# Kernel optimization log

Measured on AMD Instinct MI355X. Metric: run time of the kernel, lower is better.

The kernel has to match this reference:

```python
import jax, jax.numpy as jnp
import numpy as np

B, N, D, H = 1, 4096, 768, 12
HD = D // H
SCALE = HD ** -0.5

def setup_inputs() -> dict:
    key = jax.random.key(0)
    k1, k2, k3 = jax.random.split(key, 3)
    x = jax.random.normal(k1, (B, N, D), dtype=jnp.float32)
    W_qkv = jax.random.normal(k2, (D, 3 * D), dtype=jnp.float32) * (D ** -0.5)
    W_out = jax.random.normal(k3, (D, D), dtype=jnp.float32) * (D ** -0.5)
    b_out = jnp.zeros((D,), dtype=jnp.float32)
    return {"x": x, "W_qkv": W_qkv, "W_out": W_out, "b_out": b_out}

def reference(x, W_qkv, W_out, b_out):
    # qkv projection: (B,N,3D)
    qkv = x @ W_qkv
    q, k, v = jnp.split(qkv, 3, axis=-1)
    # (B,N,D) -> (B,H,N,hd)
    def heads(t):
        return t.reshape(B, N, H, HD).transpose(0, 2, 1, 3)
    q, k, v = heads(q), heads(k), heads(v)
    scores = jnp.einsum('bhnd,bhmd->bhnm', q, k) * SCALE  # (B,H,N,N)
    attn = jax.nn.softmax(scores, axis=-1)
    out = jnp.einsum('bhnm,bhmd->bhnd', attn, v)
    out = out.transpose(0, 2, 1, 3).reshape(B, N, D)
    return out @ W_out + b_out
```

## Files before the change

kernel.cpp:

```cpp
#include <hip/hip_runtime.h>
#include <hip/hip_bf16.h>
#include <math.h>

typedef __attribute__((ext_vector_type(8))) short bf16x8;
typedef __attribute__((ext_vector_type(4))) short bf16x4;
typedef __attribute__((ext_vector_type(4))) float floatx4;

constexpr int kN  = 4096;
constexpr int kD  = 768;
constexpr int kH  = 12;
constexpr int kHD = 64;
constexpr int k3D = 2304;
constexpr float kQScale = 0.18033688011112042f;

static __device__ __forceinline__ short f2b(float f) {
    __hip_bfloat16 h = __float2bfloat16(f);
    return *reinterpret_cast<short*>(&h);
}

static __device__ __forceinline__ float fast_exp2(float x) {
#if __has_builtin(__builtin_amdgcn_exp2f)
    return __builtin_amdgcn_exp2f(x);
#else
    return exp2f(x);
#endif
}

static __device__ __forceinline__ void async_copy16(const void* g, void* l) {
    __builtin_amdgcn_global_load_lds(
        (const __attribute__((address_space(1))) void*)g,
        (__attribute__((address_space(3))) void*)l, 16, 0, 0);
}

constexpr int kBlkX  = 1536;
constexpr int kBlkWq = 72 * 24;
constexpr int kBlkWo = 24 * 24;

__global__ __launch_bounds__(256)
void prep(const float* __restrict__ x, const float* __restrict__ Wq,
          const float* __restrict__ Wo, short* __restrict__ Xb,
          short* __restrict__ WqT, short* __restrict__ WoT)
{
    const int bid = blockIdx.x;
    const int tid = threadIdx.x;
    if (bid < kBlkX) {
        const int i = bid * 256 + tid;
        const float4* s = reinterpret_cast<const float4*>(x + (size_t)i * 8);
        float4 a = s[0], b = s[1];
        bf16x8 v;
        v[0] = f2b(a.x); v[1] = f2b(a.y); v[2] = f2b(a.z); v[3] = f2b(a.w);
        v[4] = f2b(b.x); v[5] = f2b(b.y); v[6] = f2b(b.z); v[7] = f2b(b.w);
        *reinterpret_cast<bf16x8*>(Xb + (size_t)i * 8) = v;
        return;
    }
    const float* src; short* dst; int R, C, bx, by;
    if (bid < kBlkX + kBlkWq) {
        const int local = bid - kBlkX;
        src = Wq; dst = WqT; R = kD; C = k3D; bx = local % 72; by = local / 72;
    } else {
        const int local = bid - kBlkX - kBlkWq;
        src = Wo; dst = WoT; R = kD; C = kD; bx = local % 24; by = local / 24;
    }
    __shared__ float t[32][33];
    const int c0 = bx * 32, r0 = by * 32;
    const int tx = tid & 31, ty = tid >> 5;
    #pragma unroll
    for (int i = ty; i < 32; i += 8)
        t[i][tx] = src[(size_t)(r0 + i) * C + c0 + tx];
    __syncthreads();
    #pragma unroll
    for (int i = ty; i < 32; i += 8)
        dst[(size_t)(c0 + i) * R + r0 + tx] = f2b(t[tx][i]);
}

template<int MODE>
__device__ __forceinline__
void gemm_core(const short* __restrict__ A, const short* __restrict__ BT,
               const float* __restrict__ bias, float* __restrict__ Cout,
               short* __restrict__ Qh, short* __restrict__ Kh, short* __restrict__ Vt,
               int N, int K)
{
    const int bm   = blockIdx.x * 128;
    const int bn   = blockIdx.y * 128;
    const int tid  = threadIdx.x;
    const int wave = tid >> 6;
    const int lane = tid & 63;
    const int l15  = lane & 15;
    const int quad = lane >> 4;
    const int l3   = l15 & 3;

    __shared__ alignas(16) short As[128 * 32];
    __shared__ alignas(16) short Bs[128 * 32];

    floatx4 acc[4][4] = {};
    const int wm = (wave >> 1) * 64;
    const int wn = (wave & 1) * 64;

    const int srl = lane >> 2;
    const int scc = (lane & 3) ^ (srl & 3);

    for (int k0 = 0; k0 < K; k0 += 32) {
        __syncthreads();
        #pragma unroll
        for (int j = 0; j < 2; ++j) {
            const int rs = 32 * wave + 16 * j;
            async_copy16(&A [(size_t)(bm + rs + srl) * K + k0 + 8 * scc], &As[rs * 32]);
            async_copy16(&BT[(size_t)(bn + rs + srl) * K + k0 + 8 * scc], &Bs[rs * 32]);
        }
        __syncthreads();

        bf16x8 af[4], bfr[4];
        #pragma unroll
        for (int mt = 0; mt < 4; ++mt)
            af[mt] = *reinterpret_cast<const bf16x8*>(&As[(wm + 16 * mt + l15) * 32 + 8 * (quad ^ l3)]);
        #pragma unroll
        for (int nt = 0; nt < 4; ++nt)
            bfr[nt] = *reinterpret_cast<const bf16x8*>(&Bs[(wn + 16 * nt + l15) * 32 + 8 * (quad ^ l3)]);
        #pragma unroll
        for (int mt = 0; mt < 4; ++mt)
            #pragma unroll
            for (int nt = 0; nt < 4; ++nt)
                acc[mt][nt] = __builtin_amdgcn_mfma_f32_16x16x32_bf16(af[mt], bfr[nt], acc[mt][nt], 0, 0, 0);
    }

    #pragma unroll
    for (int mt = 0; mt < 4; ++mt) {
        #pragma unroll
        for (int nt = 0; nt < 4; ++nt) {
            #pragma unroll
            for (int r = 0; r < 4; ++r) {
                const int row = bm + wm + mt * 16 + 4 * quad + r;
                const int col = bn + wn + nt * 16 + l15;
                float v = acc[mt][nt][r];
                if (MODE == 0) {
                    Cout[(size_t)row * N + col] = v + bias[col];
                } else {
                    const int proj   = col / kD;
                    const int within = col - proj * kD;
                    const int h = within >> 6;
                    const int d = within & 63;
                    if (proj == 0)      Qh[((size_t)h * kN + row) * kHD + d] = f2b(v * kQScale);
                    else if (proj == 1) Kh[((size_t)h * kN + row) * kHD + d] = f2b(v);
                    else                Vt[((size_t)h * kHD + d) * kN + row] = f2b(v);
                }
            }
        }
    }
}

__global__ __launch_bounds__(256)
void gemm_qkv(const short* __restrict__ A, const short* __restrict__ BT,
              short* __restrict__ Qh, short* __restrict__ Kh, short* __restrict__ Vt)
{
    gemm_core<1>(A, BT, nullptr, nullptr, Qh, Kh, Vt, k3D, kD);
}

__global__ __launch_bounds__(256)
void gemm_out(const short* __restrict__ A, const short* __restrict__ BT,
              const float* __restrict__ bias, float* __restrict__ Cout)
{
    gemm_core<0>(A, BT, bias, Cout, nullptr, nullptr, nullptr, kD, kD);
}

__global__ __launch_bounds__(256)
void attn(const short* __restrict__ Qh, const short* __restrict__ Kh,
          const short* __restrict__ Vt, short* __restrict__ AO)
{
    const int h    = blockIdx.y;
    const int q0   = blockIdx.x * 64;
    const int tid  = threadIdx.x;
    const int wave = tid >> 6;
    const int lane = tid & 63;
    const int l15  = lane & 15;
    const int quad = lane >> 4;
    const int lx   = l15 & 7;

    __shared__ alignas(16) short Ks[128 * 64];
    __shared__ alignas(16) short Vs[64 * 128];
    __shared__ alignas(16) short Pm[4 * 2048];

    const int qrow = q0 + 16 * wave + l15;
    const size_t qbase = ((size_t)h * kN + qrow) * kHD;
    bf16x8 qf[2];
    qf[0] = *reinterpret_cast<const bf16x8*>(&Qh[qbase + quad * 8]);
    qf[1] = *reinterpret_cast<const bf16x8*>(&Qh[qbase + 32 + quad * 8]);

    floatx4 oacc[4] = {};
    float psum = 0.f;

    const int krl = lane >> 3;
    const int kcc = (lane & 7) ^ (krl & 7);
    const int vrl = lane >> 4;
    const int vp  = lane & 15;

    short* Pw = Pm + wave * 2048;

    for (int kv0 = 0; kv0 < kN; kv0 += 128) {
        __syncthreads();
        #pragma unroll
        for (int j = 0; j < 4; ++j) {
            const int rk = 32 * wave + 8 * j;
            async_copy16(&Kh[((size_t)h * kN + kv0 + rk + krl) * kHD + 8 * kcc],
                         &Ks[rk * 64]);
            const int rv0 = 16 * wave + 4 * j;
            const int rv  = rv0 + vrl;
            async_copy16(&Vt[((size_t)h * kHD + rv) * kN + kv0 + 8 * (vp ^ (rv & 7))],
                         &Vs[rv0 * 128]);
        }
        __syncthreads();

        floatx4 sacc[8] = {};
        #pragma unroll
        for (int nt = 0; nt < 8; ++nt) {
            #pragma unroll
            for (int s = 0; s < 2; ++s) {
                bf16x8 kf = *reinterpret_cast<const bf16x8*>(
                    &Ks[(16 * nt + l15) * 64 + 8 * ((4 * s + quad) ^ lx)]);
                sacc[nt] = __builtin_amdgcn_mfma_f32_16x16x32_bf16(kf, qf[s], sacc[nt], 0, 0, 0);
            }
        }

        #pragma unroll
        for (int nt = 0; nt < 8; ++nt) {
            const float p0 = fast_exp2(sacc[nt][0]);
            const float p1 = fast_exp2(sacc[nt][1]);
            const float p2 = fast_exp2(sacc[nt][2]);
            const float p3 = fast_exp2(sacc[nt][3]);
            psum += (p0 + p1) + (p2 + p3);
            bf16x4 pk;
            pk[0] = f2b(p0); pk[1] = f2b(p1); pk[2] = f2b(p2); pk[3] = f2b(p3);
            const int c = 2 * nt + (quad >> 1);
            *reinterpret_cast<bf16x4*>(
                &Pw[l15 * 128 + 8 * (c ^ l15) + 4 * (quad & 1)]) = pk;
        }

        #pragma unroll
        for (int s = 0; s < 4; ++s) {
            bf16x8 pa = *reinterpret_cast<const bf16x8*>(
                &Pw[l15 * 128 + 8 * ((4 * s + quad) ^ l15)]);
            #pragma unroll
            for (int dt = 0; dt < 4; ++dt) {
                bf16x8 vv = *reinterpret_cast<const bf16x8*>(
                    &Vs[(16 * dt + l15) * 128 + 8 * ((4 * s + quad) ^ lx)]);
                oacc[dt] = __builtin_amdgcn_mfma_f32_16x16x32_bf16(pa, vv, oacc[dt], 0, 0, 0);
            }
        }
    }

    float v = psum;
    v += __shfl_xor(v, 16);
    v += __shfl_xor(v, 32);
    float lrow[4];
    #pragma unroll
    for (int r = 0; r < 4; ++r)
        lrow[r] = __shfl(v, 4 * quad + r);

    #pragma unroll
    for (int dt = 0; dt < 4; ++dt) {
        #pragma unroll
        for (int r = 0; r < 4; ++r) {
            const int row = q0 + 16 * wave + 4 * quad + r;
            const int col = h * kHD + 16 * dt + l15;
            AO[(size_t)row * kD + col] = f2b(oacc[dt][r] / lrow[r]);
        }
    }
}

extern "C" void kernel_launch(void* const* d_in, const int* in_sizes, int n_in,
                              void* d_out, int out_size, void* d_ws, size_t ws_size,
                              hipStream_t stream)
{
    const float* x     = (const float*)d_in[0];
    const float* W_qkv = (const float*)d_in[1];
    const float* W_out = (const float*)d_in[2];
    const float* b_out = (const float*)d_in[3];
    float* out = (float*)d_out;

    const size_t HNHD = (size_t)kH * kN * kHD;
    short* Qh    = (short*)d_ws;
    short* Kh    = Qh + HNHD;
    short* Vt    = Kh + HNHD;
    short* Xb    = Vt + HNHD;
    short* WqkvT = Xb + (size_t)kN * kD;
    short* WoutT = WqkvT + (size_t)k3D * kD;
    short* AO    = Xb;
    (void)in_sizes; (void)n_in; (void)out_size; (void)ws_size;

    prep<<<dim3(kBlkX + kBlkWq + kBlkWo), dim3(256), 0, stream>>>(
        x, W_qkv, W_out, Xb, WqkvT, WoutT);

    gemm_qkv<<<dim3(kN / 128, k3D / 128), dim3(256), 0, stream>>>(
        Xb, WqkvT, Qh, Kh, Vt);
    attn<<<dim3(kN / 64, kH), dim3(256), 0, stream>>>(Qh, Kh, Vt, AO);
    gemm_out<<<dim3(kN / 128, kD / 128), dim3(256), 0, stream>>>(
        AO, WoutT, b_out, out);
}
```

Before: 201.8 us.

## Restructure attention to 128-query tiles with split-KV waves and block swizzle

The attention kernel now handles 128 query rows per block instead of 64, so each K/V tile loaded into shared memory serves twice as many queries. The four waves are arranged 2x2: each wave owns 64 query rows and half of every 128-key tile, and the partial outputs and row sums of the two key halves are combined through shared memory at the end. Block indices are swizzled so blocks that run together share heads, and launch bounds request 3 blocks per CU. In exchange each wave holds 64 accumulator floats plus all its Q fragments in registers, and the kernel adds a reduction step at the end.

```diff
diff --git a/kernel.cpp b/kernel.cpp
--- a/kernel.cpp
+++ b/kernel.cpp
@@ -162,106 +162,167 @@
     gemm_core<0>(A, BT, bias, Cout, nullptr, nullptr, nullptr, kD, kD);
 }
 
-__global__ __launch_bounds__(256)
+__global__ __launch_bounds__(256, 3)
 void attn(const short* __restrict__ Qh, const short* __restrict__ Kh,
           const short* __restrict__ Vt, short* __restrict__ AO)
 {
-    const int h    = blockIdx.y;
-    const int q0   = blockIdx.x * 64;
+    const int flat = blockIdx.y * 32 + blockIdx.x;
+    const int W    = (flat & 7) * 48 + (flat >> 3);
+    const int h    = W >> 5;
+    const int q0   = (W & 31) * 128;
+
     const int tid  = threadIdx.x;
     const int wave = tid >> 6;
     const int lane = tid & 63;
     const int l15  = lane & 15;
     const int quad = lane >> 4;
-    const int lx   = l15 & 7;
-
-    __shared__ alignas(16) short Ks[128 * 64];
-    __shared__ alignas(16) short Vs[64 * 128];
-    __shared__ alignas(16) short Pm[4 * 2048];
-
-    const int qrow = q0 + 16 * wave + l15;
-    const size_t qbase = ((size_t)h * kN + qrow) * kHD;
-    bf16x8 qf[2];
-    qf[0] = *reinterpret_cast<const bf16x8*>(&Qh[qbase + quad * 8]);
-    qf[1] = *reinterpret_cast<const bf16x8*>(&Qh[qbase + 32 + quad * 8]);
-
-    floatx4 oacc[4] = {};
-    float psum = 0.f;
+    const int l7   = l15 & 7;
+    const int wm   = wave >> 1;
+    const int wk   = wave & 1;
+    const int swz  = (l15 >> 1) & 3;
+
+    __shared__ alignas(16) short smem[24576];
+    __shared__ float Dr[2][2][4][16];
+    short* Ks = smem;
+    short* Vs = smem + 8192;
+    short* P  = smem + 16384;
+    short* Pw = P + wave * 2048;
+
+    bf16x8 qf[4][2];
+    {
+        const size_t qb = ((size_t)h * kN + q0 + 64 * wm + l15) * kHD;
+        #pragma unroll
+        for (int mt = 0; mt < 4; ++mt)
+            #pragma unroll
+            for (int s = 0; s < 2; ++s)
+                qf[mt][s] = *reinterpret_cast<const bf16x8*>(
+                    &Qh[qb + (size_t)(16 * mt) * kHD + 32 * s + 8 * quad]);
+    }
+
+    floatx4 oacc[4][4] = {};
+    float dsum[4] = {};
 
     const int krl = lane >> 3;
-    const int kcc = (lane & 7) ^ (krl & 7);
+    const int kcc = (lane & 7) ^ krl;
     const int vrl = lane >> 4;
     const int vp  = lane & 15;
 
-    short* Pw = Pm + wave * 2048;
-
-    for (int kv0 = 0; kv0 < kN; kv0 += 128) {
+    const size_t kbase = (size_t)h * kN * kHD;
+    const size_t vbase = (size_t)h * kHD * kN;
+
+    constexpr int kNT = kN / 128;
+    for (int t = 0; t < kNT; ++t) {
+        const int kv0 = t * 128;
         __syncthreads();
         #pragma unroll
         for (int j = 0; j < 4; ++j) {
             const int rk = 32 * wave + 8 * j;
-            async_copy16(&Kh[((size_t)h * kN + kv0 + rk + krl) * kHD + 8 * kcc],
+            async_copy16(&Kh[kbase + (size_t)(kv0 + rk + krl) * kHD + 8 * kcc],
                          &Ks[rk * 64]);
             const int rv0 = 16 * wave + 4 * j;
             const int rv  = rv0 + vrl;
-            async_copy16(&Vt[((size_t)h * kHD + rv) * kN + kv0 + 8 * (vp ^ (rv & 7))],
+            async_copy16(&Vt[vbase + (size_t)rv * kN + kv0 + 8 * (vp ^ (rv & 7))],
                          &Vs[rv0 * 128]);
         }
         __syncthreads();
 
-        floatx4 sacc[8] = {};
-        #pragma unroll
-        for (int nt = 0; nt < 8; ++nt) {
-            #pragma unroll
-            for (int s = 0; s < 2; ++s) {
-                bf16x8 kf = *reinterpret_cast<const bf16x8*>(
-                    &Ks[(16 * nt + l15) * 64 + 8 * ((4 * s + quad) ^ lx)]);
-                sacc[nt] = __builtin_amdgcn_mfma_f32_16x16x32_bf16(kf, qf[s], sacc[nt], 0, 0, 0);
+        #pragma unroll
+        for (int ks = 0; ks < 2; ++ks) {
+            const int kvb = 64 * wk + 32 * ks;
+
+            #pragma unroll
+            for (int nt = 0; nt < 2; ++nt) {
+                floatx4 sacc[4] = {};
+                #pragma unroll
+                for (int s = 0; s < 2; ++s) {
+                    bf16x8 kf = *reinterpret_cast<const bf16x8*>(
+                        &Ks[(kvb + 16 * nt + l15) * 64 + 8 * ((4 * s + quad) ^ l7)]);
+                    #pragma unroll
+                    for (int mt = 0; mt < 4; ++mt)
+                        sacc[mt] = __builtin_amdgcn_mfma_f32_16x16x32_bf16(
+                            kf, qf[mt][s], sacc[mt], 0, 0, 0);
+                }
+                #pragma unroll
+                for (int mt = 0; mt < 4; ++mt) {
+                    const float p0 = fast_exp2(sacc[mt][0]);
+                    const float p1 = fast_exp2(sacc[mt][1]);
+                    const float p2 = fast_exp2(sacc[mt][2]);
+                    const float p3 = fast_exp2(sacc[mt][3]);
+                    dsum[mt] += (p0 + p1) + (p2 + p3);
+                    bf16x4 pk;
+                    pk[0] = f2b(p0); pk[1] = f2b(p1); pk[2] = f2b(p2); pk[3] = f2b(p3);
+                    *reinterpret_cast<bf16x4*>(
+                        &Pw[mt * 512 + l15 * 32 +
+                            8 * ((2 * nt + (quad >> 1)) ^ swz) + 4 * (quad & 1)]) = pk;
+                }
             }
-        }
-
-        #pragma unroll
-        for (int nt = 0; nt < 8; ++nt) {
-            const float p0 = fast_exp2(sacc[nt][0]);
-            const float p1 = fast_exp2(sacc[nt][1]);
-            const float p2 = fast_exp2(sacc[nt][2]);
-            const float p3 = fast_exp2(sacc[nt][3]);
-            psum += (p0 + p1) + (p2 + p3);
-            bf16x4 pk;
-            pk[0] = f2b(p0); pk[1] = f2b(p1); pk[2] = f2b(p2); pk[3] = f2b(p3);
-            const int c = 2 * nt + (quad >> 1);
-            *reinterpret_cast<bf16x4*>(
-                &Pw[l15 * 128 + 8 * (c ^ l15) + 4 * (quad & 1)]) = pk;
-        }
-
-        #pragma unroll
-        for (int s = 0; s < 4; ++s) {
-            bf16x8 pa = *reinterpret_cast<const bf16x8*>(
-                &Pw[l15 * 128 + 8 * ((4 * s + quad) ^ l15)]);
+
+            bf16x8 vv[4];
+            #pragma unroll
+            for (int dt = 0; dt < 4; ++dt)
+                vv[dt] = *reinterpret_cast<const bf16x8*>(
+                    &Vs[(16 * dt + l15) * 128 + 8 * ((8 * wk + 4 * ks + quad) ^ l7)]);
+            #pragma unroll
+            for (int mt = 0; mt < 4; ++mt) {
+                bf16x8 pa = *reinterpret_cast<const bf16x8*>(
+                    &Pw[mt * 512 + l15 * 32 + 8 * (quad ^ swz)]);
+                #pragma unroll
+                for (int dt = 0; dt < 4; ++dt)
+                    oacc[mt][dt] = __builtin_amdgcn_mfma_f32_16x16x32_bf16(
+                        pa, vv[dt], oacc[mt][dt], 0, 0, 0);
+            }
+        }
+    }
+
+    #pragma unroll
+    for (int mt = 0; mt < 4; ++mt) {
+        float v = dsum[mt];
+        v += __shfl_xor(v, 16);
+        v += __shfl_xor(v, 32);
+        dsum[mt] = v;
+    }
+    if (quad == 0) {
+        #pragma unroll
+        for (int mt = 0; mt < 4; ++mt)
+            Dr[wm][wk][mt][l15] = dsum[mt];
+    }
+
+    __syncthreads();
+    float* red = reinterpret_cast<float*>(smem);
+    if (wk == 1) {
+        #pragma unroll
+        for (int mt = 0; mt < 4; ++mt)
+            #pragma unroll
+            for (int dt = 0; dt < 4; ++dt)
+                *reinterpret_cast<floatx4*>(
+                    &red[wm * 4096 + (mt * 4 + dt) * 256 + l15 * 16 + quad * 4]) =
+                    oacc[mt][dt];
+    }
+    __syncthreads();
+    if (wk == 0) {
+        #pragma unroll
+        for (int mt = 0; mt < 4; ++mt) {
+            #pragma unroll
+            for (int dt = 0; dt < 4; ++dt)
+                oacc[mt][dt] += *reinterpret_cast<const floatx4*>(
+                    &red[wm * 4096 + (mt * 4 + dt) * 256 + l15 * 16 + quad * 4]);
+        }
+        #pragma unroll
+        for (int mt = 0; mt < 4; ++mt) {
+            floatx4 d0 = *reinterpret_cast<const floatx4*>(&Dr[wm][0][mt][4 * quad]);
+            floatx4 d1 = *reinterpret_cast<const floatx4*>(&Dr[wm][1][mt][4 * quad]);
+            float inv[4];
+            #pragma unroll
+            for (int r = 0; r < 4; ++r) inv[r] = 1.0f / (d0[r] + d1[r]);
             #pragma unroll
             for (int dt = 0; dt < 4; ++dt) {
-                bf16x8 vv = *reinterpret_cast<const bf16x8*>(
-                    &Vs[(16 * dt + l15) * 128 + 8 * ((4 * s + quad) ^ lx)]);
-                oacc[dt] = __builtin_amdgcn_mfma_f32_16x16x32_bf16(pa, vv, oacc[dt], 0, 0, 0);
+                #pragma unroll
+                for (int r = 0; r < 4; ++r) {
+                    const int row = q0 + 64 * wm + 16 * mt + 4 * quad + r;
+                    const int col = h * kHD + 16 * dt + l15;
+                    AO[(size_t)row * kD + col] = f2b(oacc[mt][dt][r] * inv[r]);
+                }
             }
-        }
-    }
-
-    float v = psum;
-    v += __shfl_xor(v, 16);
-    v += __shfl_xor(v, 32);
-    float lrow[4];
-    #pragma unroll
-    for (int r = 0; r < 4; ++r)
-        lrow[r] = __shfl(v, 4 * quad + r);
-
-    #pragma unroll
-    for (int dt = 0; dt < 4; ++dt) {
-        #pragma unroll
-        for (int r = 0; r < 4; ++r) {
-            const int row = q0 + 16 * wave + 4 * quad + r;
-            const int col = h * kHD + 16 * dt + l15;
-            AO[(size_t)row * kD + col] = f2b(oacc[dt][r] / lrow[r]);
         }
     }
 }
@@ -291,7 +352,7 @@
 
     gemm_qkv<<<dim3(kN / 128, k3D / 128), dim3(256), 0, stream>>>(
         Xb, WqkvT, Qh, Kh, Vt);
-    attn<<<dim3(kN / 64, kH), dim3(256), 0, stream>>>(Qh, Kh, Vt, AO);
+    attn<<<dim3(kN / 128, kH), dim3(256), 0, stream>>>(Qh, Kh, Vt, AO);
     gemm_out<<<dim3(kN / 128, kD / 128), dim3(256), 0, stream>>>(
         AO, WoutT, b_out, out);
 }
```

Measured after the change: 274.7 us. +36.1%, slower.
